# Kernel tuning notes

Hardware: AMD Instinct MI355X
Metric: run time of the kernel (lower is better)

Reference implementation:

```python
import jax, jax.numpy as jnp
import numpy as np


def prelu(x, a):
    return jnp.where(x >= 0, x, a * x)


def setup_inputs() -> dict:
    key = jax.random.key(0)
    ks = jax.random.split(key, 16)
    B, N, S, D = 4, 400, 512, 100
    rn = lambda k, shape, s=1.0: jax.random.normal(k, shape, dtype=jnp.float32) * s
    W = 0.05  # weight scale to keep activations sane
    return {
        "x": rn(ks[0], (B, N, D)),
        "G": rn(ks[1], (1, S, N), W),
        "A": rn(ks[2], (1, S, N), W),
        "W_gf": rn(ks[3], (D, N), W), "b_gf": rn(ks[4], (D,), W),
        "a_gf": jnp.float32(0.25),
        "Wg": rn(ks[5], (D, S), W), "bg": rn(ks[6], (D,), W),
        "W4a": rn(ks[7], (D, 2 * D), W), "b4a": rn(ks[8], (D,), W),
        "a4a": jnp.float32(0.25),
        "W4b": rn(ks[9], (1, D), W), "b4b": rn(ks[10], (1,), W),
        "a4b": jnp.float32(0.25),
        "W5": rn(ks[11], (D, D), W), "b5": rn(ks[12], (D,), W),
        "a5": jnp.float32(0.25),
    }


def reference(x, G, A, W_gf, b_gf, a_gf, Wg, bg, W4a, b4a, a4a, W4b, b4b, a4b, W5, b5, a5):
    B, N, D = x.shape          # (4, 400, 100)
    S = A.shape[1]             # 512
    # G1 = PReLU(Linear(G))  -> (1, S, D)
    G1 = prelu(jnp.einsum('osn,dn->osd', G, W_gf) + b_gf, a_gf)
    # A @ x -> (b, S, D)
    Ax = jnp.einsum('osn,bnd->bsd', A, x)
    # G_AX = G1 @ (A x)^T -> (b, S, S)
    G_AX = jnp.einsum('sd,btd->bst', G1[0], Ax)
    P = jax.nn.softmax(G_AX, axis=-1)                       # (b, S, S)
    # sim(): per-batch euclidean pdist on detached P
    Pd = jax.lax.stop_gradient(P)
    sq = jnp.sum(Pd * Pd, axis=-1)                          # (b, S)
    d2 = sq[:, :, None] + sq[:, None, :] - 2.0 * jnp.einsum('bij,bkj->bik', Pd, Pd)
    eye = jnp.eye(S, dtype=x.dtype)
    dist = jnp.sqrt(jnp.maximum(d2, 0.0)) * (1.0 - eye)     # squareform: zero diag
    # norm(): B = dist + I; D^-1/2 B D^-1/2; then extra .mm(B) (as in source)
    Bm = dist + eye
    dh = jnp.sum(Bm, axis=-1) ** -0.5                       # rowsum >= 1
    M = dh[:, :, None] * Bm * dh[:, None, :]
    adj = jnp.einsum('bij,bjk->bik', M, Bm)                 # (b, S, S)
    # gcn1: relu(Linear(adj @ P)), 512 -> 100
    gx = jax.nn.relu(jnp.einsum('bij,bjd->bid', adj, P) @ Wg.T + bg)  # (b, S, D)
    # tiled concat + MLP: Linear(200,100) split into x-part and gx-part
    h1 = x @ W4a[:, :D].T                                   # (b, N, D)
    h2 = gx @ W4a[:, D:].T                                  # (b, S, D)
    h = prelu(h1[:, :, None, :] + h2[:, None, :, :] + b4a, a4a)  # (b, N, S, D)
    logits = prelu(h @ W4b.T + b4b, a4b)                    # (b, N, S, 1)
    div = jax.nn.softmax(logits, axis=1)[..., 0]            # softmax over N -> (b, N, S)
    out = prelu(jnp.einsum('bns,bsd->bnd', div, gx) @ W5.T + b5, a5) + x
    return out
```

## Files before the change

### kernel.cpp

```cpp
#include <hip/hip_runtime.h>
#include <hip/hip_bf16.h>

#define BB 4
#define NN 400
#define DD 100
#define SS 512

typedef __attribute__((ext_vector_type(8))) short bf16x8;
typedef __attribute__((ext_vector_type(4))) float f32x4;

__device__ __forceinline__ float prelu_f(float v, float a) { return v >= 0.f ? v : a * v; }

__device__ __forceinline__ unsigned short f2bf(float x) {
    union { __hip_bfloat16 h; unsigned short u; } c;
    c.h = __float2bfloat16(x);
    return c.u;
}
__device__ __forceinline__ float bf2f(unsigned short u) {
    return __uint_as_float(((unsigned)u) << 16);
}

__device__ __forceinline__ bf16x8 ldfrag(const unsigned short* rowp, int grp) {
    ushort4 lo = *(const ushort4*)(rowp + grp * 4);
    ushort4 hi = *(const ushort4*)(rowp + grp * 4 + 16);
    bf16x8 r = {(short)lo.x, (short)lo.y, (short)lo.z, (short)lo.w,
                (short)hi.x, (short)hi.y, (short)hi.z, (short)hi.w};
    return r;
}

#define LPAD 136

__global__ __launch_bounds__(256)
void mmfa(const float* __restrict__ A, int lda, int sA,
          const float* __restrict__ B, int ldb, int sB, int transB,
          float* __restrict__ C, int sC, int M, int N, int K,
          int nsplit, int kchunk, int EP,
          const float* __restrict__ bias, const float* __restrict__ alpha,
          const float* __restrict__ rv, int rvStride,
          const float* __restrict__ res, int sRes)
{
    int zz = blockIdx.z;
    int b = zz / nsplit, split = zz - b * nsplit;
    int kbeg = split * kchunk, kend = min(K, kbeg + kchunk);
    int i0 = blockIdx.x * 64, n0 = blockIdx.y * 64;
    if (EP == 5 && i0 > n0) return;

    const float* Ab = A + (size_t)b * sA;
    const float* Bb = B + (size_t)b * sB;
    int tid = threadIdx.x;
    int lane = tid & 63, wave = tid >> 6;
    int r16 = lane & 15, grp = (lane >> 4) & 3;
    int wr = wave >> 1, wc = wave & 1;

    __shared__ unsigned short sa[64][LPAD];
    __shared__ unsigned short sb[64][LPAD];

    f32x4 acc[2][2];
#pragma unroll
    for (int fm = 0; fm < 2; ++fm)
#pragma unroll
        for (int fn = 0; fn < 2; ++fn)
            acc[fm][fn] = (f32x4){0.f, 0.f, 0.f, 0.f};

    for (int kt = kbeg; kt < kend; kt += 128) {
#pragma unroll
        for (int it = 0; it < 8; ++it) {
            int idx = tid + it * 256;
            int row = idx >> 5;
            int kq = (idx & 31) * 4;
            float4 v = make_float4(0.f, 0.f, 0.f, 0.f);
            if (i0 + row < M && kt + kq + 4 <= kend)
                v = *(const float4*)&Ab[(size_t)(i0 + row) * lda + kt + kq];
            ushort4 u;
            u.x = f2bf(v.x); u.y = f2bf(v.y); u.z = f2bf(v.z); u.w = f2bf(v.w);
            *(ushort4*)&sa[row][kq] = u;
        }
        if (transB) {
#pragma unroll
            for (int it = 0; it < 8; ++it) {
                int idx = tid + it * 256;
                int row = idx >> 5;
                int kq = (idx & 31) * 4;
                float4 v = make_float4(0.f, 0.f, 0.f, 0.f);
                if (n0 + row < N && kt + kq + 4 <= kend)
                    v = *(const float4*)&Bb[(size_t)(n0 + row) * ldb + kt + kq];
                ushort4 u;
                u.x = f2bf(v.x); u.y = f2bf(v.y); u.z = f2bf(v.z); u.w = f2bf(v.w);
                *(ushort4*)&sb[row][kq] = u;
            }
        } else {
#pragma unroll
            for (int it = 0; it < 8; ++it) {
                int idx = tid + it * 256;
                int kk = idx >> 4;
                int nq = (idx & 15) * 4;
                float4 v = make_float4(0.f, 0.f, 0.f, 0.f);
                if (kt + kk < kend && n0 + nq + 4 <= N)
                    v = *(const float4*)&Bb[(size_t)(kt + kk) * ldb + n0 + nq];
                sb[nq + 0][kk] = f2bf(v.x);
                sb[nq + 1][kk] = f2bf(v.y);
                sb[nq + 2][kk] = f2bf(v.z);
                sb[nq + 3][kk] = f2bf(v.w);
            }
        }
        __syncthreads();

#pragma unroll
        for (int ks = 0; ks < 4; ++ks) {
            bf16x8 a0 = ldfrag(&sa[wr * 32 + r16][ks * 32], grp);
            bf16x8 a1 = ldfrag(&sa[wr * 32 + 16 + r16][ks * 32], grp);
            bf16x8 b0 = ldfrag(&sb[wc * 32 + r16][ks * 32], grp);
            bf16x8 b1 = ldfrag(&sb[wc * 32 + 16 + r16][ks * 32], grp);
            acc[0][0] = __builtin_amdgcn_mfma_f32_16x16x32_bf16(a0, b0, acc[0][0], 0, 0, 0);
            acc[0][1] = __builtin_amdgcn_mfma_f32_16x16x32_bf16(a0, b1, acc[0][1], 0, 0, 0);
            acc[1][0] = __builtin_amdgcn_mfma_f32_16x16x32_bf16(a1, b0, acc[1][0], 0, 0, 0);
            acc[1][1] = __builtin_amdgcn_mfma_f32_16x16x32_bf16(a1, b1, acc[1][1], 0, 0, 0);
        }
        __syncthreads();
    }

    if (nsplit > 1) {
        float* Pp = C + (size_t)(b * nsplit + split) * M * N;
#pragma unroll
        for (int fm = 0; fm < 2; ++fm)
#pragma unroll
            for (int fn = 0; fn < 2; ++fn)
#pragma unroll
                for (int reg = 0; reg < 4; ++reg) {
                    int i = i0 + wr * 32 + fm * 16 + grp * 4 + reg;
                    int n = n0 + wc * 32 + fn * 16 + r16;
                    if (i < M && n < N) Pp[(size_t)i * N + n] = acc[fm][fn][reg];
                }
        return;
    }

    float al = alpha ? *alpha : 0.f;
    const float* rvb = rv ? rv + (size_t)b * rvStride : nullptr;
    float* Cb = C + (size_t)b * sC;
#pragma unroll
    for (int fm = 0; fm < 2; ++fm)
#pragma unroll
        for (int fn = 0; fn < 2; ++fn)
#pragma unroll
            for (int reg = 0; reg < 4; ++reg) {
                int i = i0 + wr * 32 + fm * 16 + grp * 4 + reg;
                int n = n0 + wc * 32 + fn * 16 + r16;
                if (i >= M || n >= N) continue;
                float v = acc[fm][fn][reg];
                if (EP == 4) {
                    v = prelu_f(v + bias[n], al) + res[(size_t)b * sRes + (size_t)i * N + n];
                } else if (EP == 5) {
                    float d2 = rvb[i] + rvb[n] - 2.f * v;
                    v = (i == n) ? 1.f : sqrtf(fmaxf(d2, 0.f));
                }
                Cb[(size_t)i * N + n] = v;
                if (EP == 5) Cb[(size_t)n * N + i] = v;
            }
}

__global__ __launch_bounds__(256)
void k_reduce(const float* __restrict__ part, int nsplit, float* __restrict__ C, int sC,
              int M, int N, int EP, const float* __restrict__ bias,
              const float* __restrict__ alpha, const float* __restrict__ rv, int rvStride)
{
    int b = blockIdx.y;
    int MN = M * N;
    int flat = (blockIdx.x * 256 + threadIdx.x) * 4;
    if (flat >= MN) return;
    const float* p = part + (size_t)b * nsplit * MN + flat;
    float4 v = *(const float4*)p;
    for (int s = 1; s < nsplit; ++s) {
        float4 w = *(const float4*)(p + (size_t)s * MN);
        v.x += w.x; v.y += w.y; v.z += w.z; v.w += w.w;
    }
    float o[4] = {v.x, v.y, v.z, v.w};
    int i = flat / N, n = flat - i * N;
    if (EP == 1) {
        float al = *alpha;
#pragma unroll
        for (int j = 0; j < 4; ++j) o[j] = prelu_f(o[j] + bias[n + j], al);
    } else if (EP == 2) {
        float r = rv[(size_t)b * rvStride + i];
#pragma unroll
        for (int j = 0; j < 4; ++j) o[j] *= r;
    } else if (EP == 3) {
        float r = rv[(size_t)b * rvStride + i];
#pragma unroll
        for (int j = 0; j < 4; ++j) { float t = r * o[j] + bias[n + j]; o[j] = t > 0.f ? t : 0.f; }
    }
    float* co = C + (size_t)b * sC + flat;
    *(float4*)co = make_float4(o[0], o[1], o[2], o[3]);
}

__global__ __launch_bounds__(512)
void k_softmax_sq(const float* __restrict__ scores, float* __restrict__ P,
                  float* __restrict__ sq)
{
    int row = blockIdx.x;
    int t = threadIdx.x;
    int w = t >> 6, lane = t & 63;
    __shared__ float sm[8];

    float v = scores[(size_t)row * SS + t];
    float m = v;
    for (int off = 32; off; off >>= 1) m = fmaxf(m, __shfl_xor(m, off, 64));
    if (lane == 0) sm[w] = m;
    __syncthreads();
    m = sm[0];
#pragma unroll
    for (int i = 1; i < 8; ++i) m = fmaxf(m, sm[i]);
    __syncthreads();

    float e = expf(v - m);
    float s = e;
    for (int off = 32; off; off >>= 1) s += __shfl_xor(s, off, 64);
    if (lane == 0) sm[w] = s;
    __syncthreads();
    s = 0.f;
#pragma unroll
    for (int i = 0; i < 8; ++i) s += sm[i];
    __syncthreads();

    float p = e / s;
    P[(size_t)row * SS + t] = p;

    float pf = bf2f(f2bf(p));
    float q = pf * pf;
    for (int off = 32; off; off >>= 1) q += __shfl_xor(q, off, 64);
    if (lane == 0) sm[w] = q;
    __syncthreads();
    if (t == 0) {
        float r = 0.f;
#pragma unroll
        for (int i = 0; i < 8; ++i) r += sm[i];
        sq[row] = r;
    }
}

__global__ __launch_bounds__(512)
void k_dh(const float* __restrict__ Bm, float* __restrict__ dh)
{
    int row = blockIdx.x;
    int t = threadIdx.x;
    int w = t >> 6, lane = t & 63;
    __shared__ float sm[8];
    float v = Bm[(size_t)row * SS + t];
    for (int off = 32; off; off >>= 1) v += __shfl_xor(v, off, 64);
    if (lane == 0) sm[w] = v;
    __syncthreads();
    if (t == 0) {
        float r = 0.f;
#pragma unroll
        for (int i = 0; i < 8; ++i) r += sm[i];
        dh[row] = rsqrtf(r);
    }
}

__global__ __launch_bounds__(256)
void k_div8(const float* __restrict__ h1, const float* __restrict__ h2,
            const float* __restrict__ b4a, const float* __restrict__ a4ap,
            const float* __restrict__ W4b, const float* __restrict__ b4bp,
            const float* __restrict__ a4bp, float* __restrict__ divT)
{
    int b = blockIdx.y;
    int s0 = blockIdx.x * 8;
    int tid = threadIdx.x;

    __shared__ float sh[8][104];
    __shared__ float sw[100];
    __shared__ float L[8][400];

    for (int idx = tid; idx < 800; idx += 256) {
        int s = idx / 100, d = idx - 100 * s;
        sh[s][d] = h2[((size_t)(b * SS + s0 + s)) * DD + d] + b4a[d];
    }
    if (tid < 100) sw[tid] = W4b[tid];
    __syncthreads();

    float a4a = *a4ap, a4b = *a4bp, b4b = *b4bp;

    for (int n = tid; n < NN; n += 256) {
        const float* h1r = &h1[((size_t)b * NN + n) * DD];
        float accs[8] = {0.f, 0.f, 0.f, 0.f, 0.f, 0.f, 0.f, 0.f};
        for (int j = 0; j < DD; j += 4) {
            float4 hv = *(const float4*)&h1r[j];
            float4 wv = *(const float4*)&sw[j];
#pragma unroll
            for (int s = 0; s < 8; ++s) {
                float4 cv = *(const float4*)&sh[s][j];
                float x0 = hv.x + cv.x; x0 = x0 > 0.f ? x0 : a4a * x0;
                float x1 = hv.y + cv.y; x1 = x1 > 0.f ? x1 : a4a * x1;
                float x2 = hv.z + cv.z; x2 = x2 > 0.f ? x2 : a4a * x2;
                float x3 = hv.w + cv.w; x3 = x3 > 0.f ? x3 : a4a * x3;
                accs[s] += x0 * wv.x + x1 * wv.y + x2 * wv.z + x3 * wv.w;
            }
        }
#pragma unroll
        for (int s = 0; s < 8; ++s) L[s][n] = prelu_f(accs[s] + b4b, a4b);
    }
    __syncthreads();

    int w = tid >> 6, lane = tid & 63;
    for (int si = w; si < 8; si += 4) {
        float m = -INFINITY;
        for (int n = lane; n < NN; n += 64) m = fmaxf(m, L[si][n]);
        for (int off = 32; off; off >>= 1) m = fmaxf(m, __shfl_xor(m, off, 64));
        float ss = 0.f;
        for (int n = lane; n < NN; n += 64) {
            float e = expf(L[si][n] - m);
            L[si][n] = e;
            ss += e;
        }
        for (int off = 32; off; off >>= 1) ss += __shfl_xor(ss, off, 64);
        float inv = 1.f / ss;
        for (int n = lane; n < NN; n += 64)
            divT[((size_t)b * NN + n) * SS + s0 + si] = L[si][n] * inv;
    }
}

extern "C" void kernel_launch(void* const* d_in, const int* in_sizes, int n_in,
                              void* d_out, int out_size, void* d_ws, size_t ws_size,
                              hipStream_t stream) {
    const float* x   = (const float*)d_in[0];
    const float* G   = (const float*)d_in[1];
    const float* Am  = (const float*)d_in[2];
    const float* Wgf = (const float*)d_in[3];
    const float* bgf = (const float*)d_in[4];
    const float* agf = (const float*)d_in[5];
    const float* Wg  = (const float*)d_in[6];
    const float* bg  = (const float*)d_in[7];
    const float* W4a = (const float*)d_in[8];
    const float* b4a = (const float*)d_in[9];
    const float* a4a = (const float*)d_in[10];
    const float* W4b = (const float*)d_in[11];
    const float* b4b = (const float*)d_in[12];
    const float* a4b = (const float*)d_in[13];
    const float* W5  = (const float*)d_in[14];
    const float* b5  = (const float*)d_in[15];
    const float* a5  = (const float*)d_in[16];
    float* out = (float*)d_out;

    float* ws  = (float*)d_ws;
    float* G1  = ws;
    float* Ax  = ws + 51200;
    float* P   = ws + 256000;
    float* BmS = ws + 1304576;
    float* sq  = ws + 2353152;
    float* dh  = ws + 2355200;
    float* PW  = ws + 2357248;
    float* T1s = ws + 2562048;
    float* gx  = ws + 2766848;
    float* h1  = ws + 2971648;
    float* h2  = ws + 3131648;
    float* tmp = ws + 3336448;
    float* divT  = P;
    float* part  = h1;
    float* partP = P;
    float* partB = BmS;

    mmfa<<<dim3(8, 2, 2), 256, 0, stream>>>(G, NN, 0, Wgf, NN, 0, 1,
        part, 0, SS, DD, NN, 2, 200, 0, nullptr, nullptr, nullptr, 0, nullptr, 0);
    k_reduce<<<dim3(50, 1), 256, 0, stream>>>(part, 2, G1, SS * DD, SS, DD, 1, bgf, agf, nullptr, 0);
    mmfa<<<dim3(8, 2, 2 * BB), 256, 0, stream>>>(Am, NN, 0, x, DD, NN * DD, 0,
        part, 0, SS, DD, NN, 2, 200, 0, nullptr, nullptr, nullptr, 0, nullptr, 0);
    k_reduce<<<dim3(50, BB), 256, 0, stream>>>(part, 2, Ax, SS * DD, SS, DD, 0, nullptr, nullptr, nullptr, 0);
    mmfa<<<dim3(8, 8, BB), 256, 0, stream>>>(G1, DD, 0, Ax, DD, SS * DD, 1,
        BmS, SS * SS, SS, SS, DD, 1, DD, 0, nullptr, nullptr, nullptr, 0, nullptr, 0);
    k_softmax_sq<<<BB * SS, 512, 0, stream>>>(BmS, P, sq);
    mmfa<<<dim3(8, 8, BB), 256, 0, stream>>>(P, SS, SS * SS, P, SS, SS * SS, 1,
        BmS, SS * SS, SS, SS, SS, 1, SS, 5, nullptr, nullptr, sq, SS, nullptr, 0);
    k_dh<<<BB * SS, 512, 0, stream>>>(BmS, dh);
    mmfa<<<dim3(8, 2, 2 * BB), 256, 0, stream>>>(P, SS, SS * SS, Wg, SS, 0, 1,
        part, 0, SS, DD, SS, 2, 256, 0, nullptr, nullptr, nullptr, 0, nullptr, 0);
    k_reduce<<<dim3(50, BB), 256, 0, stream>>>(part, 2, PW, SS * DD, SS, DD, 0, nullptr, nullptr, nullptr, 0);
    mmfa<<<dim3(8, 2, 2 * BB), 256, 0, stream>>>(BmS, SS, SS * SS, PW, DD, SS * DD, 0,
        partP, 0, SS, DD, SS, 2, 256, 0, nullptr, nullptr, nullptr, 0, nullptr, 0);
    k_reduce<<<dim3(50, BB), 256, 0, stream>>>(partP, 2, T1s, SS * DD, SS, DD, 2, nullptr, nullptr, dh, SS);
    mmfa<<<dim3(8, 2, 2 * BB), 256, 0, stream>>>(BmS, SS, SS * SS, T1s, DD, SS * DD, 0,
        partP, 0, SS, DD, SS, 2, 256, 0, nullptr, nullptr, nullptr, 0, nullptr, 0);
    k_reduce<<<dim3(50, BB), 256, 0, stream>>>(partP, 2, gx, SS * DD, SS, DD, 3, bg, nullptr, dh, SS);
    mmfa<<<dim3(7, 2, BB), 256, 0, stream>>>(x, DD, NN * DD, W4a, 2 * DD, 0, 1,
        h1, NN * DD, NN, DD, DD, 1, DD, 0, nullptr, nullptr, nullptr, 0, nullptr, 0);
    mmfa<<<dim3(8, 2, BB), 256, 0, stream>>>(gx, DD, SS * DD, W4a + DD, 2 * DD, 0, 1,
        h2, SS * DD, SS, DD, DD, 1, DD, 0, nullptr, nullptr, nullptr, 0, nullptr, 0);
    k_div8<<<dim3(SS / 8, BB), 256, 0, stream>>>(h1, h2, b4a, a4a, W4b, b4b, a4b, divT);
    mmfa<<<dim3(7, 2, 2 * BB), 256, 0, stream>>>(divT, SS, NN * SS, gx, DD, SS * DD, 0,
        partB, 0, NN, DD, SS, 2, 256, 0, nullptr, nullptr, nullptr, 0, nullptr, 0);
    k_reduce<<<dim3(40, BB), 256, 0, stream>>>(partB, 2, tmp, NN * DD, NN, DD, 0, nullptr, nullptr, nullptr, 0);
    mmfa<<<dim3(7, 2, BB), 256, 0, stream>>>(tmp, DD, NN * DD, W5, DD, 0, 1,
        out, NN * DD, NN, DD, DD, 1, DD, 4, b5, a5, nullptr, 0, x, NN * DD);
}
```

Baseline: 293.4 us.

## Fuse pipeline into persistent cooperative kernel with grid syncs and bf16 P

Replaces the ~19 separate kernel launches with one cooperative persistent kernel of 256 blocks that walks through phases separated by grid-wide syncs. Split-K partial buffers and their reduce kernels are dropped, so epilogues are applied directly in the tile routine. P is stored as bf16 and loaded without conversion, and independent GEMMs (G1/Ax/h1, gram/PW) are merged into shared phases. This removes launch gaps and reduction traffic, at the cost of lower parallelism per GEMM and the overhead of each grid barrier. A multi-launch path is kept as fallback if the cooperative launch fails.

Measured after the change: 578.0 us. +97.0%, slower.

```diff
diff --git a/kernel.cpp b/kernel.cpp
--- a/kernel.cpp
+++ b/kernel.cpp
@@ -1,10 +1,15 @@
 #include <hip/hip_runtime.h>
 #include <hip/hip_bf16.h>
+#include <hip/hip_cooperative_groups.h>
+
+namespace cg = cooperative_groups;
 
 #define BB 4
 #define NN 400
 #define DD 100
 #define SS 512
+#define LPAD 136
+#define GRID 256
 
 typedef __attribute__((ext_vector_type(8))) short bf16x8;
 typedef __attribute__((ext_vector_type(4))) float f32x4;
@@ -28,33 +33,44 @@
     return r;
 }
 
-#define LPAD 136
-
-__global__ __launch_bounds__(256)
-void mmfa(const float* __restrict__ A, int lda, int sA,
-          const float* __restrict__ B, int ldb, int sB, int transB,
-          float* __restrict__ C, int sC, int M, int N, int K,
-          int nsplit, int kchunk, int EP,
-          const float* __restrict__ bias, const float* __restrict__ alpha,
-          const float* __restrict__ rv, int rvStride,
-          const float* __restrict__ res, int sRes)
+struct KP {
+    const float *x, *G, *Am, *Wgf, *bgf, *agf, *Wg, *bg, *W4a, *b4a, *a4a,
+                *W4b, *b4b, *a4b, *W5, *b5, *a5;
+    float* out;
+    float* ws;
+};
+
+#define OFS_G1  0
+#define OFS_AX  51200
+#define OFS_SC  256000
+#define OFS_SQ  1304576
+#define OFS_DH  1306624
+#define OFS_PW  1308672
+#define OFS_T1  1513472
+#define OFS_GX  1718272
+#define OFS_H1  1923072
+#define OFS_H2  2083072
+#define OFS_DV  2287872
+#define OFS_TMP 3107072
+#define OFS_PB  3267072
+
+#define SMEM_BYTES (64 * LPAD * 2 * 2)
+
+__device__ void mm_tile(char* smemraw,
+                        const void* Ap, int aBf, int lda,
+                        const void* Bp, int bBf, int ldb, int transB,
+                        int i0, int n0, int M, int N, int K,
+                        float* C, int ldc, int EP,
+                        const float* bias, const float* alphaP,
+                        const float* rv, const float* res, int resLd)
 {
-    int zz = blockIdx.z;
-    int b = zz / nsplit, split = zz - b * nsplit;
-    int kbeg = split * kchunk, kend = min(K, kbeg + kchunk);
-    int i0 = blockIdx.x * 64, n0 = blockIdx.y * 64;
-    if (EP == 5 && i0 > n0) return;
-
-    const float* Ab = A + (size_t)b * sA;
-    const float* Bb = B + (size_t)b * sB;
+    unsigned short (*sa)[LPAD] = (unsigned short(*)[LPAD])smemraw;
+    unsigned short (*sb)[LPAD] = (unsigned short(*)[LPAD])(smemraw + 64 * LPAD * 2);
     int tid = threadIdx.x;
     int lane = tid & 63, wave = tid >> 6;
     int r16 = lane & 15, grp = (lane >> 4) & 3;
     int wr = wave >> 1, wc = wave & 1;
 
-    __shared__ unsigned short sa[64][LPAD];
-    __shared__ unsigned short sb[64][LPAD];
-
     f32x4 acc[2][2];
 #pragma unroll
     for (int fm = 0; fm < 2; ++fm)
@@ -62,40 +78,68 @@
         for (int fn = 0; fn < 2; ++fn)
             acc[fm][fn] = (f32x4){0.f, 0.f, 0.f, 0.f};
 
-    for (int kt = kbeg; kt < kend; kt += 128) {
-#pragma unroll
-        for (int it = 0; it < 8; ++it) {
-            int idx = tid + it * 256;
-            int row = idx >> 5;
-            int kq = (idx & 31) * 4;
-            float4 v = make_float4(0.f, 0.f, 0.f, 0.f);
-            if (i0 + row < M && kt + kq + 4 <= kend)
-                v = *(const float4*)&Ab[(size_t)(i0 + row) * lda + kt + kq];
-            ushort4 u;
-            u.x = f2bf(v.x); u.y = f2bf(v.y); u.z = f2bf(v.z); u.w = f2bf(v.w);
-            *(ushort4*)&sa[row][kq] = u;
-        }
-        if (transB) {
+    __syncthreads();
+    for (int kt = 0; kt < K; kt += 128) {
+        if (aBf) {
+            const unsigned short* Ab = (const unsigned short*)Ap;
 #pragma unroll
             for (int it = 0; it < 8; ++it) {
                 int idx = tid + it * 256;
-                int row = idx >> 5;
-                int kq = (idx & 31) * 4;
+                int row = idx >> 5, kq = (idx & 31) * 4;
+                ushort4 u = {0, 0, 0, 0};
+                if (i0 + row < M && kt + kq + 4 <= K)
+                    u = *(const ushort4*)&Ab[(size_t)(i0 + row) * lda + kt + kq];
+                *(ushort4*)&sa[row][kq] = u;
+            }
+        } else {
+            const float* Ab = (const float*)Ap;
+#pragma unroll
+            for (int it = 0; it < 8; ++it) {
+                int idx = tid + it * 256;
+                int row = idx >> 5, kq = (idx & 31) * 4;
                 float4 v = make_float4(0.f, 0.f, 0.f, 0.f);
-                if (n0 + row < N && kt + kq + 4 <= kend)
-                    v = *(const float4*)&Bb[(size_t)(n0 + row) * ldb + kt + kq];
+                if (i0 + row < M && kt + kq + 4 <= K)
+                    v = *(const float4*)&Ab[(size_t)(i0 + row) * lda + kt + kq];
                 ushort4 u;
                 u.x = f2bf(v.x); u.y = f2bf(v.y); u.z = f2bf(v.z); u.w = f2bf(v.w);
-                *(ushort4*)&sb[row][kq] = u;
+                *(ushort4*)&sa[row][kq] = u;
+            }
+        }
+        if (transB) {
+            if (bBf) {
+                const unsigned short* Bb = (const unsigned short*)Bp;
+#pragma unroll
+                for (int it = 0; it < 8; ++it) {
+                    int idx = tid + it * 256;
+                    int row = idx >> 5, kq = (idx & 31) * 4;
+                    ushort4 u = {0, 0, 0, 0};
+                    if (n0 + row < N && kt + kq + 4 <= K)
+                        u = *(const ushort4*)&Bb[(size_t)(n0 + row) * ldb + kt + kq];
+                    *(ushort4*)&sb[row][kq] = u;
+                }
+            } else {
+                const float* Bb = (const float*)Bp;
+#pragma unroll
+                for (int it = 0; it < 8; ++it) {
+                    int idx = tid + it * 256;
+                    int row = idx >> 5, kq = (idx & 31) * 4;
+                    float4 v = make_float4(0.f, 0.f, 0.f, 0.f);
+                    if (n0 + row < N && kt + kq + 4 <= K)
+                        v = *(const float4*)&Bb[(size_t)(n0 + row) * ldb + kt + kq];
+                    ushort4 u;
+                    u.x = f2bf(v.x); u.y = f2bf(v.y); u.z = f2bf(v.z); u.w = f2bf(v.w);
+                    *(ushort4*)&sb[row][kq] = u;
+                }
             }
         } else {
+            const float* Bb = (const float*)Bp;
 #pragma unroll
             for (int it = 0; it < 8; ++it) {
                 int idx = tid + it * 256;
                 int kk = idx >> 4;
                 int nq = (idx & 15) * 4;
                 float4 v = make_float4(0.f, 0.f, 0.f, 0.f);
-                if (kt + kk < kend && n0 + nq + 4 <= N)
+                if (kt + kk < K && n0 + nq + 4 <= N)
                     v = *(const float4*)&Bb[(size_t)(kt + kk) * ldb + n0 + nq];
                 sb[nq + 0][kk] = f2bf(v.x);
                 sb[nq + 1][kk] = f2bf(v.y);
@@ -104,7 +148,6 @@
             }
         }
         __syncthreads();
-
 #pragma unroll
         for (int ks = 0; ks < 4; ++ks) {
             bf16x8 a0 = ldfrag(&sa[wr * 32 + r16][ks * 32], grp);
@@ -119,24 +162,7 @@
         __syncthreads();
     }
 
-    if (nsplit > 1) {
-        float* Pp = C + (size_t)(b * nsplit + split) * M * N;
-#pragma unroll
-        for (int fm = 0; fm < 2; ++fm)
-#pragma unroll
-            for (int fn = 0; fn < 2; ++fn)
-#pragma unroll
-                for (int reg = 0; reg < 4; ++reg) {
-                    int i = i0 + wr * 32 + fm * 16 + grp * 4 + reg;
-                    int n = n0 + wc * 32 + fn * 16 + r16;
-                    if (i < M && n < N) Pp[(size_t)i * N + n] = acc[fm][fn][reg];
-                }
-        return;
-    }
-
-    float al = alpha ? *alpha : 0.f;
-    const float* rvb = rv ? rv + (size_t)b * rvStride : nullptr;
-    float* Cb = C + (size_t)b * sC;
+    float al = alphaP ? *alphaP : 0.f;
 #pragma unroll
     for (int fm = 0; fm < 2; ++fm)
 #pragma unroll
@@ -147,147 +173,198 @@
                 int n = n0 + wc * 32 + fn * 16 + r16;
                 if (i >= M || n >= N) continue;
                 float v = acc[fm][fn][reg];
-                if (EP == 4) {
-                    v = prelu_f(v + bias[n], al) + res[(size_t)b * sRes + (size_t)i * N + n];
-                } else if (EP == 5) {
-                    float d2 = rvb[i] + rvb[n] - 2.f * v;
+                if (EP == 1) v = prelu_f(v + bias[n], al);
+                else if (EP == 2) v *= rv[i];
+                else if (EP == 3) { float t = rv[i] * v + bias[n]; v = t > 0.f ? t : 0.f; }
+                else if (EP == 4) v = prelu_f(v + bias[n], al) + res[(size_t)i * resLd + n];
+                else if (EP == 5) {
+                    float d2 = rv[i] + rv[n] - 2.f * v;
                     v = (i == n) ? 1.f : sqrtf(fmaxf(d2, 0.f));
                 }
-                Cb[(size_t)i * N + n] = v;
-                if (EP == 5) Cb[(size_t)n * N + i] = v;
-            }
-}
-
-__global__ __launch_bounds__(256)
-void k_reduce(const float* __restrict__ part, int nsplit, float* __restrict__ C, int sC,
-              int M, int N, int EP, const float* __restrict__ bias,
-              const float* __restrict__ alpha, const float* __restrict__ rv, int rvStride)
-{
-    int b = blockIdx.y;
-    int MN = M * N;
-    int flat = (blockIdx.x * 256 + threadIdx.x) * 4;
-    if (flat >= MN) return;
-    const float* p = part + (size_t)b * nsplit * MN + flat;
-    float4 v = *(const float4*)p;
-    for (int s = 1; s < nsplit; ++s) {
-        float4 w = *(const float4*)(p + (size_t)s * MN);
-        v.x += w.x; v.y += w.y; v.z += w.z; v.w += w.w;
-    }
-    float o[4] = {v.x, v.y, v.z, v.w};
-    int i = flat / N, n = flat - i * N;
-    if (EP == 1) {
-        float al = *alpha;
-#pragma unroll
-        for (int j = 0; j < 4; ++j) o[j] = prelu_f(o[j] + bias[n + j], al);
-    } else if (EP == 2) {
-        float r = rv[(size_t)b * rvStride + i];
-#pragma unroll
-        for (int j = 0; j < 4; ++j) o[j] *= r;
-    } else if (EP == 3) {
-        float r = rv[(size_t)b * rvStride + i];
-#pragma unroll
-        for (int j = 0; j < 4; ++j) { float t = r * o[j] + bias[n + j]; o[j] = t > 0.f ? t : 0.f; }
-    }
-    float* co = C + (size_t)b * sC + flat;
-    *(float4*)co = make_float4(o[0], o[1], o[2], o[3]);
-}
-
-__global__ __launch_bounds__(512)
-void k_softmax_sq(const float* __restrict__ scores, float* __restrict__ P,
-                  float* __restrict__ sq)
-{
-    int row = blockIdx.x;
-    int t = threadIdx.x;
-    int w = t >> 6, lane = t & 63;
-    __shared__ float sm[8];
-
-    float v = scores[(size_t)row * SS + t];
-    float m = v;
-    for (int off = 32; off; off >>= 1) m = fmaxf(m, __shfl_xor(m, off, 64));
-    if (lane == 0) sm[w] = m;
-    __syncthreads();
-    m = sm[0];
-#pragma unroll
-    for (int i = 1; i < 8; ++i) m = fmaxf(m, sm[i]);
-    __syncthreads();
-
-    float e = expf(v - m);
-    float s = e;
-    for (int off = 32; off; off >>= 1) s += __shfl_xor(s, off, 64);
-    if (lane == 0) sm[w] = s;
-    __syncthreads();
-    s = 0.f;
-#pragma unroll
-    for (int i = 0; i < 8; ++i) s += sm[i];
-    __syncthreads();
-
-    float p = e / s;
-    P[(size_t)row * SS + t] = p;
-
-    float pf = bf2f(f2bf(p));
-    float q = pf * pf;
-    for (int off = 32; off; off >>= 1) q += __shfl_xor(q, off, 64);
-    if (lane == 0) sm[w] = q;
-    __syncthreads();
-    if (t == 0) {
-        float r = 0.f;
-#pragma unroll
-        for (int i = 0; i < 8; ++i) r += sm[i];
-        sq[row] = r;
-    }
-}
-
-__global__ __launch_bounds__(512)
-void k_dh(const float* __restrict__ Bm, float* __restrict__ dh)
-{
-    int row = blockIdx.x;
-    int t = threadIdx.x;
-    int w = t >> 6, lane = t & 63;
-    __shared__ float sm[8];
-    float v = Bm[(size_t)row * SS + t];
-    for (int off = 32; off; off >>= 1) v += __shfl_xor(v, off, 64);
-    if (lane == 0) sm[w] = v;
-    __syncthreads();
-    if (t == 0) {
-        float r = 0.f;
-#pragma unroll
-        for (int i = 0; i < 8; ++i) r += sm[i];
-        dh[row] = rsqrtf(r);
-    }
-}
-
-__global__ __launch_bounds__(256)
-void k_div8(const float* __restrict__ h1, const float* __restrict__ h2,
-            const float* __restrict__ b4a, const float* __restrict__ a4ap,
-            const float* __restrict__ W4b, const float* __restrict__ b4bp,
-            const float* __restrict__ a4bp, float* __restrict__ divT)
-{
-    int b = blockIdx.y;
-    int s0 = blockIdx.x * 8;
+                C[(size_t)i * ldc + n] = v;
+                if (EP == 5) C[(size_t)n * ldc + i] = v;
+            }
+}
+
+
+__device__ void phase_pre(const KP& p, char* sm) {
+    float* G1 = p.ws + OFS_G1;
+    float* Ax = p.ws + OFS_AX;
+    float* h1 = p.ws + OFS_H1;
+    for (int t = blockIdx.x; t < 136; t += gridDim.x) {
+        if (t < 16) {
+            int it = t >> 1, nt = t & 1;
+            mm_tile(sm, p.G, 0, NN, p.Wgf, 0, NN, 1, it * 64, nt * 64, SS, DD, NN,
+                    G1, DD, 1, p.bgf, p.agf, nullptr, nullptr, 0);
+        } else if (t < 80) {
+            int u = t - 16, b = u >> 4, r = u & 15, it = r >> 1, nt = r & 1;
+            mm_tile(sm, p.Am, 0, NN, p.x + (size_t)b * NN * DD, 0, DD, 0,
+                    it * 64, nt * 64, SS, DD, NN,
+                    Ax + (size_t)b * SS * DD, DD, 0, nullptr, nullptr, nullptr, nullptr, 0);
+        } else {
+            int u = t - 80, b = u / 14, r = u % 14, it = r >> 1, nt = r & 1;
+            mm_tile(sm, p.x + (size_t)b * NN * DD, 0, DD, p.W4a, 0, 2 * DD, 1,
+                    it * 64, nt * 64, NN, DD, DD,
+                    h1 + (size_t)b * NN * DD, DD, 0, nullptr, nullptr, nullptr, nullptr, 0);
+        }
+    }
+}
+
+__device__ void phase_scores(const KP& p, char* sm) {
+    float* G1 = p.ws + OFS_G1;
+    float* Ax = p.ws + OFS_AX;
+    float* sc = p.ws + OFS_SC;
+    for (int t = blockIdx.x; t < 256; t += gridDim.x) {
+        int b = t >> 6, r = t & 63, it = r >> 3, nt = r & 7;
+        mm_tile(sm, G1, 0, DD, Ax + (size_t)b * SS * DD, 0, DD, 1,
+                it * 64, nt * 64, SS, SS, DD,
+                sc + (size_t)b * SS * SS, SS, 0, nullptr, nullptr, nullptr, nullptr, 0);
+    }
+}
+
+__device__ void phase_softmax(const KP& p, char* sm) {
+    float* sc = p.ws + OFS_SC;
+    float* sq = p.ws + OFS_SQ;
+    unsigned short* Pb = (unsigned short*)(p.ws + OFS_PB);
+    float* red = (float*)sm;
+    int tid = threadIdx.x, lane = tid & 63, wave = tid >> 6;
+    __syncthreads();
+    for (int r8 = 0; r8 < 8; ++r8) {
+        int row = blockIdx.x * 8 + r8;
+        const float* srow = sc + (size_t)row * SS;
+        float v0 = srow[tid], v1 = srow[tid + 256];
+        float m = fmaxf(v0, v1);
+        for (int off = 32; off; off >>= 1) m = fmaxf(m, __shfl_xor(m, off, 64));
+        if (lane == 0) red[wave] = m;
+        __syncthreads();
+        m = fmaxf(fmaxf(red[0], red[1]), fmaxf(red[2], red[3]));
+        __syncthreads();
+        float e0 = expf(v0 - m), e1 = expf(v1 - m);
+        float s = e0 + e1;
+        for (int off = 32; off; off >>= 1) s += __shfl_xor(s, off, 64);
+        if (lane == 0) red[wave] = s;
+        __syncthreads();
+        s = red[0] + red[1] + red[2] + red[3];
+        __syncthreads();
+        float inv = 1.f / s;
+        unsigned short u0 = f2bf(e0 * inv), u1 = f2bf(e1 * inv);
+        Pb[(size_t)row * SS + tid] = u0;
+        Pb[(size_t)row * SS + tid + 256] = u1;
+        float p0 = bf2f(u0), p1 = bf2f(u1);
+        float q = p0 * p0 + p1 * p1;
+        for (int off = 32; off; off >>= 1) q += __shfl_xor(q, off, 64);
+        if (lane == 0) red[wave] = q;
+        __syncthreads();
+        if (tid == 0) sq[row] = red[0] + red[1] + red[2] + red[3];
+        __syncthreads();
+    }
+}
+
+__device__ void phase_gram(const KP& p, char* sm) {
+    float* Bm = p.ws + OFS_SC;
+    float* sq = p.ws + OFS_SQ;
+    float* PW = p.ws + OFS_PW;
+    unsigned short* Pb = (unsigned short*)(p.ws + OFS_PB);
+    for (int t = blockIdx.x; t < 208; t += gridDim.x) {
+        if (t < 144) {
+            int b = t / 36, r = t % 36, it = 0, nt = 0;
+            for (it = 0; it < 8; ++it) { int cnt = 8 - it; if (r < cnt) { nt = it + r; break; } r -= cnt; }
+            mm_tile(sm, Pb + (size_t)b * SS * SS, 1, SS, Pb + (size_t)b * SS * SS, 1, SS, 1,
+                    it * 64, nt * 64, SS, SS, SS,
+                    Bm + (size_t)b * SS * SS, SS, 5, nullptr, nullptr, sq + (size_t)b * SS, nullptr, 0);
+        } else {
+            int u = t - 144, b = u >> 4, r = u & 15, it = r >> 1, nt = r & 1;
+            mm_tile(sm, Pb + (size_t)b * SS * SS, 1, SS, p.Wg, 0, SS, 1,
+                    it * 64, nt * 64, SS, DD, SS,
+                    PW + (size_t)b * SS * DD, DD, 0, nullptr, nullptr, nullptr, nullptr, 0);
+        }
+    }
+}
+
+__device__ void phase_dh(const KP& p, char* sm) {
+    float* Bm = p.ws + OFS_SC;
+    float* dh = p.ws + OFS_DH;
+    float* red = (float*)sm;
+    int tid = threadIdx.x, lane = tid & 63, wave = tid >> 6;
+    __syncthreads();
+    for (int r8 = 0; r8 < 8; ++r8) {
+        int row = blockIdx.x * 8 + r8;
+        const float* brow = Bm + (size_t)row * SS;
+        float v = brow[tid] + brow[tid + 256];
+        for (int off = 32; off; off >>= 1) v += __shfl_xor(v, off, 64);
+        if (lane == 0) red[wave] = v;
+        __syncthreads();
+        if (tid == 0) dh[row] = rsqrtf(red[0] + red[1] + red[2] + red[3]);
+        __syncthreads();
+    }
+}
+
+__device__ void phase_t1(const KP& p, char* sm) {
+    float* Bm = p.ws + OFS_SC;
+    float* PW = p.ws + OFS_PW;
+    float* T1 = p.ws + OFS_T1;
+    float* dh = p.ws + OFS_DH;
+    for (int t = blockIdx.x; t < 64; t += gridDim.x) {
+        int b = t >> 4, r = t & 15, it = r >> 1, nt = r & 1;
+        mm_tile(sm, Bm + (size_t)b * SS * SS, 0, SS, PW + (size_t)b * SS * DD, 0, DD, 0,
+                it * 64, nt * 64, SS, DD, SS,
+                T1 + (size_t)b * SS * DD, DD, 2, nullptr, nullptr, dh + (size_t)b * SS, nullptr, 0);
+    }
+}
+
+__device__ void phase_gx(const KP& p, char* sm) {
+    float* Bm = p.ws + OFS_SC;
+    float* T1 = p.ws + OFS_T1;
+    float* gx = p.ws + OFS_GX;
+    float* dh = p.ws + OFS_DH;
+    for (int t = blockIdx.x; t < 64; t += gridDim.x) {
+        int b = t >> 4, r = t & 15, it = r >> 1, nt = r & 1;
+        mm_tile(sm, Bm + (size_t)b * SS * SS, 0, SS, T1 + (size_t)b * SS * DD, 0, DD, 0,
+                it * 64, nt * 64, SS, DD, SS,
+                gx + (size_t)b * SS * DD, DD, 3, p.bg, nullptr, dh + (size_t)b * SS, nullptr, 0);
+    }
+}
+
+__device__ void phase_h2(const KP& p, char* sm) {
+    float* gx = p.ws + OFS_GX;
+    float* h2 = p.ws + OFS_H2;
+    for (int t = blockIdx.x; t < 64; t += gridDim.x) {
+        int b = t >> 4, r = t & 15, it = r >> 1, nt = r & 1;
+        mm_tile(sm, gx + (size_t)b * SS * DD, 0, DD, p.W4a + DD, 0, 2 * DD, 1,
+                it * 64, nt * 64, SS, DD, DD,
+                h2 + (size_t)b * SS * DD, DD, 0, nullptr, nullptr, nullptr, nullptr, 0);
+    }
+}
+
+struct DivS { float sh[8][104]; float sw[104]; float L[8][400]; };
+
+__device__ void phase_div(const KP& p, char* sm) {
+    float* h1 = p.ws + OFS_H1;
+    float* h2 = p.ws + OFS_H2;
+    float* dv = p.ws + OFS_DV;
+    DivS* sd = (DivS*)sm;
+    int b = blockIdx.x >> 6;
+    int s0 = (blockIdx.x & 63) * 8;
     int tid = threadIdx.x;
-
-    __shared__ float sh[8][104];
-    __shared__ float sw[100];
-    __shared__ float L[8][400];
-
+    __syncthreads();
     for (int idx = tid; idx < 800; idx += 256) {
         int s = idx / 100, d = idx - 100 * s;
-        sh[s][d] = h2[((size_t)(b * SS + s0 + s)) * DD + d] + b4a[d];
-    }
-    if (tid < 100) sw[tid] = W4b[tid];
-    __syncthreads();
-
-    float a4a = *a4ap, a4b = *a4bp, b4b = *b4bp;
+        sd->sh[s][d] = h2[((size_t)(b * SS + s0 + s)) * DD + d] + p.b4a[d];
+    }
+    if (tid < 100) sd->sw[tid] = p.W4b[tid];
+    __syncthreads();
+
+    float a4a = *p.a4a, a4b = *p.a4b, b4b = *p.b4b;
 
     for (int n = tid; n < NN; n += 256) {
         const float* h1r = &h1[((size_t)b * NN + n) * DD];
         float accs[8] = {0.f, 0.f, 0.f, 0.f, 0.f, 0.f, 0.f, 0.f};
         for (int j = 0; j < DD; j += 4) {
             float4 hv = *(const float4*)&h1r[j];
-            float4 wv = *(const float4*)&sw[j];
+            float4 wv = *(const float4*)&sd->sw[j];
 #pragma unroll
             for (int s = 0; s < 8; ++s) {
-                float4 cv = *(const float4*)&sh[s][j];
+                float4 cv = *(const float4*)&sd->sh[s][j];
                 float x0 = hv.x + cv.x; x0 = x0 > 0.f ? x0 : a4a * x0;
                 float x1 = hv.y + cv.y; x1 = x1 > 0.f ? x1 : a4a * x1;
                 float x2 = hv.z + cv.z; x2 = x2 > 0.f ? x2 : a4a * x2;
@@ -296,97 +373,123 @@
             }
         }
 #pragma unroll
-        for (int s = 0; s < 8; ++s) L[s][n] = prelu_f(accs[s] + b4b, a4b);
+        for (int s = 0; s < 8; ++s) sd->L[s][n] = prelu_f(accs[s] + b4b, a4b);
     }
     __syncthreads();
 
     int w = tid >> 6, lane = tid & 63;
     for (int si = w; si < 8; si += 4) {
         float m = -INFINITY;
-        for (int n = lane; n < NN; n += 64) m = fmaxf(m, L[si][n]);
+        for (int n = lane; n < NN; n += 64) m = fmaxf(m, sd->L[si][n]);
         for (int off = 32; off; off >>= 1) m = fmaxf(m, __shfl_xor(m, off, 64));
         float ss = 0.f;
         for (int n = lane; n < NN; n += 64) {
-            float e = expf(L[si][n] - m);
-            L[si][n] = e;
+            float e = expf(sd->L[si][n] - m);
+            sd->L[si][n] = e;
             ss += e;
         }
         for (int off = 32; off; off >>= 1) ss += __shfl_xor(ss, off, 64);
         float inv = 1.f / ss;
         for (int n = lane; n < NN; n += 64)
-            divT[((size_t)b * NN + n) * SS + s0 + si] = L[si][n] * inv;
-    }
-}
+            dv[((size_t)b * NN + n) * SS + s0 + si] = sd->L[si][n] * inv;
+    }
+    __syncthreads();
+}
+
+__device__ void phase_tmp(const KP& p, char* sm) {
+    float* dv  = p.ws + OFS_DV;
+    float* gx  = p.ws + OFS_GX;
+    float* tmp = p.ws + OFS_TMP;
+    for (int t = blockIdx.x; t < 56; t += gridDim.x) {
+        int b = t / 14, r = t % 14, it = r >> 1, nt = r & 1;
+        mm_tile(sm, dv + (size_t)b * NN * SS, 0, SS, gx + (size_t)b * SS * DD, 0, DD, 0,
+                it * 64, nt * 64, NN, DD, SS,
+                tmp + (size_t)b * NN * DD, DD, 0, nullptr, nullptr, nullptr, nullptr, 0);
+    }
+}
+
+__device__ void phase_out(const KP& p, char* sm) {
+    float* tmp = p.ws + OFS_TMP;
+    for (int t = blockIdx.x; t < 56; t += gridDim.x) {
+        int b = t / 14, r = t % 14, it = r >> 1, nt = r & 1;
+        mm_tile(sm, tmp + (size_t)b * NN * DD, 0, DD, p.W5, 0, DD, 1,
+                it * 64, nt * 64, NN, DD, DD,
+                p.out + (size_t)b * NN * DD, DD, 4, p.b5, p.a5,
+                nullptr, p.x + (size_t)b * NN * DD, DD);
+    }
+}
+
+__global__ __launch_bounds__(256)
+void persist(KP p) {
+    __shared__ __align__(16) char sm[SMEM_BYTES];
+    cg::grid_group g = cg::this_grid();
+    phase_pre(p, sm);      g.sync();
+    phase_scores(p, sm);   g.sync();
+    phase_softmax(p, sm);  g.sync();
+    phase_gram(p, sm);     g.sync();
+    phase_dh(p, sm);       g.sync();
+    phase_t1(p, sm);       g.sync();
+    phase_gx(p, sm);       g.sync();
+    phase_h2(p, sm);       g.sync();
+    phase_div(p, sm);      g.sync();
+    phase_tmp(p, sm);      g.sync();
+    phase_out(p, sm);
+}
+
+#define PHASE_KERNEL(name, fn) \
+    __global__ __launch_bounds__(256) void name(KP p) { \
+        __shared__ __align__(16) char sm[SMEM_BYTES]; fn(p, sm); }
+PHASE_KERNEL(kPre, phase_pre)
+PHASE_KERNEL(kScores, phase_scores)
+PHASE_KERNEL(kSoftmax, phase_softmax)
+PHASE_KERNEL(kGram, phase_gram)
+PHASE_KERNEL(kDh, phase_dh)
+PHASE_KERNEL(kT1, phase_t1)
+PHASE_KERNEL(kGx, phase_gx)
+PHASE_KERNEL(kH2, phase_h2)
+PHASE_KERNEL(kDiv, phase_div)
+PHASE_KERNEL(kTmp, phase_tmp)
+PHASE_KERNEL(kOut, phase_out)
 
 extern "C" void kernel_launch(void* const* d_in, const int* in_sizes, int n_in,
                               void* d_out, int out_size, void* d_ws, size_t ws_size,
                               hipStream_t stream) {
-    const float* x   = (const float*)d_in[0];
-    const float* G   = (const float*)d_in[1];
-    const float* Am  = (const float*)d_in[2];
-    const float* Wgf = (const float*)d_in[3];
-    const float* bgf = (const float*)d_in[4];
-    const float* agf = (const float*)d_in[5];
-    const float* Wg  = (const float*)d_in[6];
-    const float* bg  = (const float*)d_in[7];
-    const float* W4a = (const float*)d_in[8];
-    const float* b4a = (const float*)d_in[9];
-    const float* a4a = (const float*)d_in[10];
-    const float* W4b = (const float*)d_in[11];
-    const float* b4b = (const float*)d_in[12];
-    const float* a4b = (const float*)d_in[13];
-    const float* W5  = (const float*)d_in[14];
-    const float* b5  = (const float*)d_in[15];
-    const float* a5  = (const float*)d_in[16];
-    float* out = (float*)d_out;
-
-    float* ws  = (float*)d_ws;
-    float* G1  = ws;
-    float* Ax  = ws + 51200;
-    float* P   = ws + 256000;
-    float* BmS = ws + 1304576;
-    float* sq  = ws + 2353152;
-    float* dh  = ws + 2355200;
-    float* PW  = ws + 2357248;
-    float* T1s = ws + 2562048;
-    float* gx  = ws + 2766848;
-    float* h1  = ws + 2971648;
-    float* h2  = ws + 3131648;
-    float* tmp = ws + 3336448;
-    float* divT  = P;
-    float* part  = h1;
-    float* partP = P;
-    float* partB = BmS;
-
-    mmfa<<<dim3(8, 2, 2), 256, 0, stream>>>(G, NN, 0, Wgf, NN, 0, 1,
-        part, 0, SS, DD, NN, 2, 200, 0, nullptr, nullptr, nullptr, 0, nullptr, 0);
-    k_reduce<<<dim3(50, 1), 256, 0, stream>>>(part, 2, G1, SS * DD, SS, DD, 1, bgf, agf, nullptr, 0);
-    mmfa<<<dim3(8, 2, 2 * BB), 256, 0, stream>>>(Am, NN, 0, x, DD, NN * DD, 0,
-        part, 0, SS, DD, NN, 2, 200, 0, nullptr, nullptr, nullptr, 0, nullptr, 0);
-    k_reduce<<<dim3(50, BB), 256, 0, stream>>>(part, 2, Ax, SS * DD, SS, DD, 0, nullptr, nullptr, nullptr, 0);
-    mmfa<<<dim3(8, 8, BB), 256, 0, stream>>>(G1, DD, 0, Ax, DD, SS * DD, 1,
-        BmS, SS * SS, SS, SS, DD, 1, DD, 0, nullptr, nullptr, nullptr, 0, nullptr, 0);
-    k_softmax_sq<<<BB * SS, 512, 0, stream>>>(BmS, P, sq);
-    mmfa<<<dim3(8, 8, BB), 256, 0, stream>>>(P, SS, SS * SS, P, SS, SS * SS, 1,
-        BmS, SS * SS, SS, SS, SS, 1, SS, 5, nullptr, nullptr, sq, SS, nullptr, 0);
-    k_dh<<<BB * SS, 512, 0, stream>>>(BmS, dh);
-    mmfa<<<dim3(8, 2, 2 * BB), 256, 0, stream>>>(P, SS, SS * SS, Wg, SS, 0, 1,
-        part, 0, SS, DD, SS, 2, 256, 0, nullptr, nullptr, nullptr, 0, nullptr, 0);
-    k_reduce<<<dim3(50, BB), 256, 0, stream>>>(part, 2, PW, SS * DD, SS, DD, 0, nullptr, nullptr, nullptr, 0);
-    mmfa<<<dim3(8, 2, 2 * BB), 256, 0, stream>>>(BmS, SS, SS * SS, PW, DD, SS * DD, 0,
-        partP, 0, SS, DD, SS, 2, 256, 0, nullptr, nullptr, nullptr, 0, nullptr, 0);
-    k_reduce<<<dim3(50, BB), 256, 0, stream>>>(partP, 2, T1s, SS * DD, SS, DD, 2, nullptr, nullptr, dh, SS);
-    mmfa<<<dim3(8, 2, 2 * BB), 256, 0, stream>>>(BmS, SS, SS * SS, T1s, DD, SS * DD, 0,
-        partP, 0, SS, DD, SS, 2, 256, 0, nullptr, nullptr, nullptr, 0, nullptr, 0);
-    k_reduce<<<dim3(50, BB), 256, 0, stream>>>(partP, 2, gx, SS * DD, SS, DD, 3, bg, nullptr, dh, SS);
-    mmfa<<<dim3(7, 2, BB), 256, 0, stream>>>(x, DD, NN * DD, W4a, 2 * DD, 0, 1,
-        h1, NN * DD, NN, DD, DD, 1, DD, 0, nullptr, nullptr, nullptr, 0, nullptr, 0);
-    mmfa<<<dim3(8, 2, BB), 256, 0, stream>>>(gx, DD, SS * DD, W4a + DD, 2 * DD, 0, 1,
-        h2, SS * DD, SS, DD, DD, 1, DD, 0, nullptr, nullptr, nullptr, 0, nullptr, 0);
-    k_div8<<<dim3(SS / 8, BB), 256, 0, stream>>>(h1, h2, b4a, a4a, W4b, b4b, a4b, divT);
-    mmfa<<<dim3(7, 2, 2 * BB), 256, 0, stream>>>(divT, SS, NN * SS, gx, DD, SS * DD, 0,
-        partB, 0, NN, DD, SS, 2, 256, 0, nullptr, nullptr, nullptr, 0, nullptr, 0);
-    k_reduce<<<dim3(40, BB), 256, 0, stream>>>(partB, 2, tmp, NN * DD, NN, DD, 0, nullptr, nullptr, nullptr, 0);
-    mmfa<<<dim3(7, 2, BB), 256, 0, stream>>>(tmp, DD, NN * DD, W5, DD, 0, 1,
-        out, NN * DD, NN, DD, DD, 1, DD, 4, b5, a5, nullptr, 0, x, NN * DD);
-}
+    KP kp;
+    kp.x   = (const float*)d_in[0];
+    kp.G   = (const float*)d_in[1];
+    kp.Am  = (const float*)d_in[2];
+    kp.Wgf = (const float*)d_in[3];
+    kp.bgf = (const float*)d_in[4];
+    kp.agf = (const float*)d_in[5];
+    kp.Wg  = (const float*)d_in[6];
+    kp.bg  = (const float*)d_in[7];
+    kp.W4a = (const float*)d_in[8];
+    kp.b4a = (const float*)d_in[9];
+    kp.a4a = (const float*)d_in[10];
+    kp.W4b = (const float*)d_in[11];
+    kp.b4b = (const float*)d_in[12];
+    kp.a4b = (const float*)d_in[13];
+    kp.W5  = (const float*)d_in[14];
+    kp.b5  = (const float*)d_in[15];
+    kp.a5  = (const float*)d_in[16];
+    kp.out = (float*)d_out;
+    kp.ws  = (float*)d_ws;
+
+    void* args[] = { (void*)&kp };
+    hipError_t err = hipLaunchCooperativeKernel((const void*)persist,
+                                                dim3(GRID), dim3(256), args, 0, stream);
+    if (err != hipSuccess) {
+        (void)hipGetLastError();
+        kPre<<<GRID, 256, 0, stream>>>(kp);
+        kScores<<<GRID, 256, 0, stream>>>(kp);
+        kSoftmax<<<GRID, 256, 0, stream>>>(kp);
+        kGram<<<GRID, 256, 0, stream>>>(kp);
+        kDh<<<GRID, 256, 0, stream>>>(kp);
+        kT1<<<GRID, 256, 0, stream>>>(kp);
+        kGx<<<GRID, 256, 0, stream>>>(kp);
+        kH2<<<GRID, 256, 0, stream>>>(kp);
+        kDiv<<<GRID, 256, 0, stream>>>(kp);
+        kTmp<<<GRID, 256, 0, stream>>>(kp);
+        kOut<<<GRID, 256, 0, stream>>>(kp);
+    }
+}
```
